# Performance work log

Measured on AMD Instinct MI355X. Metric: run time of the kernel, lower is better.

The kernel has to match this reference:

```python
import jax, jax.numpy as jnp
import numpy as np

HIDDEN = 2048
N_HEADS = 32
N_KV = 8
HEAD_DIM = 128
EPS = 1e-6
THETA = 10000.0
WINDOW = 512
T = 2048


def _rms_norm(x, w, eps=EPS):
    # x: [..., d]
    var = jnp.mean(x * x, axis=-1, keepdims=True)
    return x * jax.lax.rsqrt(var + eps) * w


def _rope(x, positions):
    # neox-style full rotary, x: [T, H, d]
    d = x.shape[-1]
    inv_freq = 1.0 / (THETA ** (jnp.arange(0, d, 2, dtype=jnp.float32) / d))  # [d/2]
    ang = positions.astype(jnp.float32)[:, None] * inv_freq  # [T, d/2]
    cos = jnp.cos(ang)[:, None, :]  # [T,1,d/2]
    sin = jnp.sin(ang)[:, None, :]
    x1, x2 = x[..., : d // 2], x[..., d // 2 :]
    return jnp.concatenate([x1 * cos - x2 * sin, x2 * cos + x1 * sin], axis=-1)


def setup_inputs() -> dict:
    key = jax.random.key(0)
    ks = jax.random.split(key, 6)
    q_size = N_HEADS * HEAD_DIM
    kv_size = N_KV * HEAD_DIM
    s = 1.0 / np.sqrt(HIDDEN)
    return {
        "positions": jnp.arange(T, dtype=jnp.int32),
        "hidden_states": jax.random.normal(ks[0], (T, HIDDEN), dtype=jnp.float32),
        "w_qkv": jax.random.normal(ks[1], (HIDDEN, q_size + 2 * kv_size), dtype=jnp.float32) * s,
        "w_o": jax.random.normal(ks[2], (q_size, HIDDEN), dtype=jnp.float32) * s,
        "w_g": jax.random.normal(ks[3], (HIDDEN, N_HEADS), dtype=jnp.float32) * s,
        "q_norm_w": jnp.ones((HEAD_DIM,), dtype=jnp.float32),
        "k_norm_w": jnp.ones((HEAD_DIM,), dtype=jnp.float32),
    }


def reference(positions, hidden_states, w_qkv, w_o, w_g, q_norm_w, k_norm_w):
    t = hidden_states.shape[0]
    q_size = N_HEADS * HEAD_DIM
    kv_size = N_KV * HEAD_DIM
    scale = HEAD_DIM ** -0.5
    group = N_HEADS // N_KV

    qkv = hidden_states @ w_qkv  # [T, q+2kv]
    q = qkv[:, :q_size].reshape(t, N_HEADS, HEAD_DIM)
    k = qkv[:, q_size : q_size + kv_size].reshape(t, N_KV, HEAD_DIM)
    v = qkv[:, q_size + kv_size :].reshape(t, N_KV, HEAD_DIM)

    # per-head RMSNorm then RoPE
    q = _rope(_rms_norm(q, q_norm_w), positions)
    k = _rope(_rms_norm(k, k_norm_w), positions)

    # sliding-window causal attention with GQA (group queries per kv head)
    qg = q.reshape(t, N_KV, group, HEAD_DIM)
    scores = jnp.einsum("tkgd,skd->kgts", qg, k) * scale  # [Hkv,G,T,T]
    diff = positions[:, None] - positions[None, :]  # i - j
    mask = (diff >= 0) & (diff < WINDOW)  # causal + sliding window
    scores = jnp.where(mask[None, None], scores, -jnp.inf)
    probs = jax.nn.softmax(scores, axis=-1)
    attn = jnp.einsum("kgts,skd->tkgd", probs, v).reshape(t, N_HEADS, HEAD_DIM)

    # softplus gate per head, then output projection
    gate = jax.nn.softplus((hidden_states @ w_g).astype(jnp.float32)).astype(attn.dtype)
    attn = attn * gate[:, :, None]
    return attn.reshape(t, q_size) @ w_o
```

## Files before the change

kernel.cpp:

```cpp
#include <hip/hip_runtime.h>

typedef __attribute__((ext_vector_type(4))) float floatx4;
typedef __attribute__((ext_vector_type(8))) _Float16 half8;
typedef __attribute__((ext_vector_type(4))) _Float16 half4;

#define TT 2048
#define HIDDEN 2048
#define NH 32
#define NKV 8
#define HD 128
#define QSIZE 4096
#define KVSIZE 1024
#define QKVN 6144
#define WQR 6400
#define GOFF 6144
#define QKSTR 5120
#define WINDOW 512

__global__ __launch_bounds__(256) void prep_kernel(
    const float* __restrict__ w_qkv, const float* __restrict__ w_o,
    const float* __restrict__ hidden, const float* __restrict__ w_g,
    const int* __restrict__ positions,
    _Float16* __restrict__ Wqkvt, _Float16* __restrict__ Wot,
    _Float16* __restrict__ Xb, float* __restrict__ tbl) {
  __shared__ float tile[64][68];
  int bid = blockIdx.x;
  int tid = threadIdx.x;
  if (bid >= 5120) {
    if (bid < 7168) {
      int i = ((bid - 5120) * 256 + tid) * 8;
      float4 a = *(const float4*)&hidden[i];
      float4 b = *(const float4*)&hidden[i + 4];
      alignas(16) _Float16 o[8] = {(_Float16)a.x, (_Float16)a.y, (_Float16)a.z, (_Float16)a.w,
                                   (_Float16)b.x, (_Float16)b.y, (_Float16)b.z, (_Float16)b.w};
      *(uint4*)&Xb[i] = *(const uint4*)o;
    } else if (bid < 7392) {
      int i = ((bid - 7168) * 256 + tid) * 8;
      *(uint4*)&Wqkvt[(size_t)(GOFF + NH) * HIDDEN + i] = (uint4){0, 0, 0, 0};
    } else if (bid < 7456) {
      int br = (bid - 7392) * 32;
      int c = tid & 31, r0 = tid >> 5;
      __shared__ float gt[32][33];
#pragma unroll
      for (int i = 0; i < 4; ++i) {
        int r = r0 + 8 * i;
        gt[r][c] = w_g[(size_t)(br + r) * NH + c];
      }
      __syncthreads();
#pragma unroll
      for (int i = 0; i < 4; ++i) {
        int r = r0 + 8 * i;
        Wqkvt[(size_t)(GOFF + r) * HIDDEN + br + c] = (_Float16)gt[c][r];
      }
    } else {
      int idx = (bid - 7456) * 256 + tid;
      int t = idx >> 6, j = idx & 63;
      float pos = (float)positions[t];
      float invf = exp2f(-(float)j * (13.287712379549449f / 64.0f));
      float sn, cs;
      sincosf(pos * invf, &sn, &cs);
      tbl[t * 128 + j] = cs;
      tbl[t * 128 + 64 + j] = sn;
    }
    return;
  }
  const float* in;
  _Float16* out;
  int R, C, tilesX, t;
  if (bid < 3072) { in = w_qkv; out = Wqkvt; R = HIDDEN; C = QKVN; tilesX = 96; t = bid; }
  else           { in = w_o;   out = Wot;   R = QSIZE;  C = HIDDEN; tilesX = 32; t = bid - 3072; }
  int bc = (t % tilesX) * 64, br = (t / tilesX) * 64;
  int rr = tid >> 4, l16 = tid & 15;
#pragma unroll
  for (int it = 0; it < 4; ++it) {
    int r = rr + it * 16;
    *(float4*)&tile[r][l16 * 4] = *(const float4*)&in[(size_t)(br + r) * C + bc + l16 * 4];
  }
  __syncthreads();
  int orow = tid >> 2, rr0 = (tid & 3) * 16;
  alignas(16) _Float16 tmp[16];
#pragma unroll
  for (int jj = 0; jj < 16; ++jj) tmp[jj] = (_Float16)tile[rr0 + jj][orow];
  *(uint4*)&out[(size_t)(bc + orow) * R + br + rr0] = *(const uint4*)&tmp[0];
  *(uint4*)&out[(size_t)(bc + orow) * R + br + rr0 + 8] = *(const uint4*)&tmp[8];
}

__device__ __forceinline__ void async16(const _Float16* g, _Float16* l) {
  __builtin_amdgcn_global_load_lds((const __attribute__((address_space(1))) void*)g,
                                   (__attribute__((address_space(3))) void*)l, 16, 0, 0);
}

#define G256_K 2048

#define STG_A(ob, mh, kt)                                                        \
  async16(As0 + (size_t)(mh) * 64 * G256_K + (kt), &lds[(ob) + ((mh) * 64 + r0A0) * 64]); \
  async16(As1 + (size_t)(mh) * 64 * G256_K + (kt), &lds[(ob) + ((mh) * 64 + r0A1) * 64]);
#define STG_B(ob, nh, kt)                                                        \
  async16(Bs0 + (size_t)(nh) * 32 * G256_K + (kt), &lds[(ob) + 16384 + ((nh) * 32 + r0B0) * 64]); \
  async16(Bs1 + (size_t)(nh) * 32 * G256_K + (kt), &lds[(ob) + 16384 + ((nh) * 32 + r0B1) * 64]);

#define LD_A(DST, mh)                                                            \
  _Pragma("unroll") for (int fm = 0; fm < 4; ++fm)                               \
  _Pragma("unroll") for (int ks = 0; ks < 2; ++ks)                               \
    DST[fm][ks] = *(const half8*)&LA[(wm * 128 + (mh) * 64 + fm * 16 + lr) * 64 + \
                                     (((ks * 4 + quad) ^ l7) * 8)];
#define LD_B(DST, nh)                                                            \
  _Pragma("unroll") for (int fn = 0; fn < 2; ++fn)                               \
  _Pragma("unroll") for (int ks = 0; ks < 2; ++ks)                               \
    DST[fn][ks] = *(const half8*)&LB[(wn * 64 + (nh) * 32 + fn * 16 + lr) * 64 + \
                                     (((ks * 4 + quad) ^ l7) * 8)];
#define MFMAQ(AS, BS, mh, nh)                                                    \
  __builtin_amdgcn_s_setprio(1);                                                 \
  _Pragma("unroll") for (int fm = 0; fm < 4; ++fm)                               \
  _Pragma("unroll") for (int fn = 0; fn < 2; ++fn)                               \
  _Pragma("unroll") for (int ks = 0; ks < 2; ++ks)                               \
    acc[(mh) * 4 + fm][(nh) * 2 + fn] = __builtin_amdgcn_mfma_f32_16x16x32_f16(  \
        AS[fm][ks], BS[fn][ks], acc[(mh) * 4 + fm][(nh) * 2 + fn], 0, 0, 0);     \
  __builtin_amdgcn_s_setprio(0);
#define VMW0 asm volatile("s_waitcnt vmcnt(0)" ::: "memory")
#define BAR __builtin_amdgcn_s_barrier()
#define SB0 __builtin_amdgcn_sched_barrier(0)

__global__ __launch_bounds__(512, 2) void gemm256_kernel(
    const _Float16* __restrict__ A, const _Float16* __restrict__ Bt,
    _Float16* __restrict__ QKb, _Float16* __restrict__ Vf,
    _Float16* __restrict__ Gate) {
  __shared__ _Float16 lds[65536];
  int tid = threadIdx.x;
  int wave = tid >> 6, lane = tid & 63;
  int wm = wave >> 2, wn = wave & 3;
  int lr = lane & 15, quad = lane >> 4, l7 = lane & 7, l3 = lane >> 3;
  int m0 = blockIdx.x * 256, n0 = blockIdx.y * 256;

  int q0 = wave * 2, q1 = q0 + 1;
  int r0A0 = (q0 >> 3) * 128 + (q0 & 7) * 8;
  int r0A1 = (q1 >> 3) * 128 + (q1 & 7) * 8;
  int r0B0 = (q0 >> 2) * 64 + (q0 & 3) * 8;
  int r0B1 = (q1 >> 2) * 64 + (q1 & 3) * 8;
  int gA8 = (l7 ^ l3) * 8;

  const _Float16* As0 = A + (size_t)(m0 + r0A0 + l3) * G256_K + gA8;
  const _Float16* As1 = A + (size_t)(m0 + r0A1 + l3) * G256_K + gA8;
  const _Float16* Bs0 = Bt + (size_t)(n0 + r0B0 + l3) * G256_K + gA8;
  const _Float16* Bs1 = Bt + (size_t)(n0 + r0B1 + l3) * G256_K + gA8;

  floatx4 acc[8][4];
#pragma unroll
  for (int i = 0; i < 8; ++i)
#pragma unroll
    for (int j = 0; j < 4; ++j) acc[i][j] = (floatx4){0.f, 0.f, 0.f, 0.f};

  STG_A(0, 0, 0);
  STG_A(0, 1, 0);
  STG_B(0, 0, 0);
  STG_B(0, 1, 0);
  VMW0;
  BAR;
  SB0;

  half8 a0f[4][2], a1f[4][2], b0[2][2], b1[2][2];

  for (int t = 0; t < 32; ++t) {
    int bb = (t & 1) << 15;
    int ob = bb ^ 32768;
    int ktn = (t + 1) * 64;
    bool stg = (t < 31);
    const _Float16* LA = &lds[bb];
    const _Float16* LB = &lds[bb + 16384];

    if (stg) {
      STG_A(ob, 0, ktn);
      STG_B(ob, 0, ktn);
      STG_B(ob, 1, ktn);
      STG_A(ob, 1, ktn);
    }

    LD_B(b0, 0);
    LD_A(a0f, 0);
    MFMAQ(a0f, b0, 0, 0);
    LD_B(b1, 1);
    MFMAQ(a0f, b1, 0, 1);
    LD_A(a1f, 1);
    MFMAQ(a1f, b0, 1, 0);
    MFMAQ(a1f, b1, 1, 1);

    if (stg) VMW0;
    BAR;
    SB0;
  }

  int nt = blockIdx.y;
  if (nt < 20) {
#pragma unroll
    for (int mh = 0; mh < 2; ++mh)
#pragma unroll
      for (int fm = 0; fm < 4; ++fm)
#pragma unroll
        for (int nh = 0; nh < 2; ++nh)
#pragma unroll
          for (int fn = 0; fn < 2; ++fn)
#pragma unroll
            for (int rr = 0; rr < 4; ++rr) {
              int row = m0 + wm * 128 + mh * 64 + fm * 16 + quad * 4 + rr;
              int col = nt * 256 + wn * 64 + nh * 32 + fn * 16 + lr;
              QKb[(size_t)row * QKSTR + col] = (_Float16)acc[mh * 4 + fm][nh * 2 + fn][rr];
            }
  } else if (nt < 24) {
#pragma unroll
    for (int mh = 0; mh < 2; ++mh)
#pragma unroll
      for (int fm = 0; fm < 4; ++fm)
#pragma unroll
        for (int nh = 0; nh < 2; ++nh)
#pragma unroll
          for (int fn = 0; fn < 2; ++fn)
#pragma unroll
            for (int rq = 0; rq < 4; ++rq) {
              int row = fm * 16 + quad * 4 + rq;
              int t = m0 + wm * 128 + mh * 64 + row;
              int cg = wn * 64 + nh * 32 + fn * 16 + lr;
              int kh = (nt - 20) * 2 + (cg >> 7);
              int d = cg & 127;
              int sv = t & 63;
              _Float16* vb = Vf + ((size_t)kh * 32 + (t >> 6)) * 8192;
              int c = (d >> 4) * 128 + (sv >> 5) * 64 + ((sv >> 3) & 3) * 16 + (d & 15);
              vb[c * 8 + (sv & 7)] = (_Float16)acc[mh * 4 + fm][nh * 2 + fn][rq];
            }
  } else {
    if (wn == 0) {
#pragma unroll
      for (int mh = 0; mh < 2; ++mh)
#pragma unroll
        for (int fm = 0; fm < 4; ++fm)
#pragma unroll
          for (int fn = 0; fn < 2; ++fn)
#pragma unroll
            for (int rq = 0; rq < 4; ++rq) {
              int row = fm * 16 + quad * 4 + rq;
              int t = m0 + wm * 128 + mh * 64 + row;
              int col = fn * 16 + lr;
              Gate[(size_t)t * NH + col] = (_Float16)acc[mh * 4 + fm][fn][rq];
            }
    }
  }
}

__global__ __launch_bounds__(256) void normrope_k_kernel(
    const _Float16* __restrict__ QKb, const float* __restrict__ kw,
    const float* __restrict__ tbl, _Float16* __restrict__ Kf) {
  int wid = blockIdx.x * 4 + (threadIdx.x >> 6);
  int lane = threadIdx.x & 63;
  int t = wid >> 3, hh = wid & 7;
  const _Float16* src = QKb + (size_t)t * QKSTR + QSIZE + hh * HD;
  float x1 = (float)src[lane];
  float x2 = (float)src[lane + 64];
  float ss = x1 * x1 + x2 * x2;
#pragma unroll
  for (int off = 1; off < 64; off <<= 1) ss += __shfl_xor(ss, off);
  float rr = rsqrtf(ss * (1.0f / 128.0f) + 1e-6f);
  float n1 = x1 * rr * kw[lane];
  float n2 = x2 * rr * kw[lane + 64];
  float cs = tbl[(size_t)t * 128 + lane];
  float sn = tbl[(size_t)t * 128 + 64 + lane];
  float r1 = n1 * cs - n2 * sn;
  float r2 = n2 * cs + n1 * sn;
  int st = t >> 6, jt = (t >> 4) & 3, n16 = t & 15;
  _Float16* kb = Kf + (size_t)(hh * 32 + st) * 8192;
  int c = jt * 256 + (lane >> 5) * 64 + ((lane >> 3) & 3) * 16 + n16;
  kb[c * 8 + (lane & 7)] = (_Float16)r1;
  kb[(c + 128) * 8 + (lane & 7)] = (_Float16)r2;
}

__device__ __forceinline__ void swizzle_mn(int& m0, int& n0) {
  int ntiles = gridDim.y;
  int pid = blockIdx.x + blockIdx.y * gridDim.x;
  int band = pid / (8 * ntiles);
  int wi = pid - band * (8 * ntiles);
  m0 = (band * 8 + (wi & 7)) * 128;
  n0 = (wi >> 3) * 128;
}

__global__ __launch_bounds__(256, 2) void gemm_bt_splitk_kernel(
    const _Float16* __restrict__ A, const _Float16* __restrict__ Bt,
    float* __restrict__ Cp, int M, int N, int K, int Ks) {
  __shared__ _Float16 As[128 * 64];
  __shared__ _Float16 Bs[128 * 64];
  int tid = threadIdx.x;
  int wave = tid >> 6, lane = tid & 63;
  int wm = wave >> 1, wn = wave & 1;
  int m0, n0;
  swizzle_mn(m0, n0);
  int kb = blockIdx.z * Ks;
  float* C = Cp + (size_t)blockIdx.z * M * N;
  int lr = lane & 15;
  int quad = lane >> 4;
  floatx4 acc[4][4];
#pragma unroll
  for (int i = 0; i < 4; ++i)
#pragma unroll
    for (int j = 0; j < 4; ++j) acc[i][j] = (floatx4){0.f, 0.f, 0.f, 0.f};

  for (int k0 = kb; k0 < kb + Ks; k0 += 64) {
    __syncthreads();
#pragma unroll
    for (int it = 0; it < 4; ++it) {
      int c = tid + it * 256;
      int row = c >> 3, j = c & 7;
      int jj = j ^ (row & 7);
      _Float16* la = &As[it * 2048 + wave * 512];
      _Float16* lb = &Bs[it * 2048 + wave * 512];
      async16(&A[(size_t)(m0 + row) * K + k0 + jj * 8], la);
      async16(&Bt[(size_t)(n0 + row) * K + k0 + jj * 8], lb);
    }
    __syncthreads();
#pragma unroll
    for (int kc = 0; kc < 2; ++kc) {
      int ch = kc * 4 + quad;
      half8 a[4], b[4];
#pragma unroll
      for (int i = 0; i < 4; ++i) {
        int r = wm * 64 + i * 16 + lr;
        a[i] = *(const half8*)&As[r * 64 + (ch ^ (r & 7)) * 8];
      }
#pragma unroll
      for (int j = 0; j < 4; ++j) {
        int r = wn * 64 + j * 16 + lr;
        b[j] = *(const half8*)&Bs[r * 64 + (ch ^ (r & 7)) * 8];
      }
#pragma unroll
      for (int i = 0; i < 4; ++i)
#pragma unroll
        for (int j = 0; j < 4; ++j)
          acc[i][j] = __builtin_amdgcn_mfma_f32_16x16x32_f16(a[i], b[j], acc[i][j], 0, 0, 0);
    }
  }
  int rq = quad * 4;
#pragma unroll
  for (int i = 0; i < 4; ++i)
#pragma unroll
    for (int j = 0; j < 4; ++j)
#pragma unroll
      for (int r = 0; r < 4; ++r) {
        int row = m0 + wm * 64 + i * 16 + rq + r;
        int col = n0 + wn * 64 + j * 16 + lr;
        C[(size_t)row * N + col] = acc[i][j][r];
      }
}

__global__ __launch_bounds__(256) void reduce2_kernel(const float* __restrict__ P,
                                                      float* __restrict__ out) {
  size_t i = ((size_t)blockIdx.x * 256 + threadIdx.x) * 8;
  const float* Q = P + (size_t)TT * HIDDEN;
  float4 a0 = *(const float4*)&P[i];
  float4 a1 = *(const float4*)&P[i + 4];
  float4 b0 = *(const float4*)&Q[i];
  float4 b1 = *(const float4*)&Q[i + 4];
  a0.x += b0.x; a0.y += b0.y; a0.z += b0.z; a0.w += b0.w;
  a1.x += b1.x; a1.y += b1.y; a1.z += b1.z; a1.w += b1.w;
  *(float4*)&out[i] = a0;
  *(float4*)&out[i + 4] = a1;
}

#define PSTR 68
#define M0 8.0f
__global__ __launch_bounds__(256, 2) void attn_kernel(
    const _Float16* __restrict__ QKb, const float* __restrict__ qw,
    const float* __restrict__ tbl, const _Float16* __restrict__ Kf,
    const _Float16* __restrict__ Vf, const _Float16* __restrict__ Gate,
    _Float16* __restrict__ Og) {
  const float scale = 0.08838834764831845f;
  __shared__ _Float16 Ps[4][16 * PSTR];
  int tid = threadIdx.x;
  int wave = tid >> 6, lane = tid & 63;
  int n16 = lane & 15, quad = lane >> 4;
  int t0 = blockIdx.x * 16;
  int kh = blockIdx.y;
  int h = kh * 4 + wave;
  _Float16* ps = Ps[wave];

  half8 qf[4];
  {
    int tq = t0 + n16;
    half8 rq[4];
#pragma unroll
    for (int kc = 0; kc < 4; ++kc)
      rq[kc] = *(const half8*)&QKb[(size_t)tq * QKSTR + h * HD + kc * 32 + quad * 8];
    float x[4][8];
    float ss = 0.f;
#pragma unroll
    for (int kc = 0; kc < 4; ++kc)
#pragma unroll
      for (int j = 0; j < 8; ++j) {
        x[kc][j] = (float)rq[kc][j];
        ss += x[kc][j] * x[kc][j];
      }
    ss += __shfl_xor(ss, 16);
    ss += __shfl_xor(ss, 32);
    float inv = rsqrtf(ss * (1.0f / 128.0f) + 1e-6f);
#pragma unroll
    for (int kc = 0; kc < 2; ++kc) {
      int d0 = kc * 32 + quad * 8;
      const float* tb = &tbl[(size_t)tq * 128 + d0];
      const float* w1 = &qw[d0];
      const float* w2 = &qw[d0 + 64];
#pragma unroll
      for (int j = 0; j < 8; ++j) {
        float cs = tb[j], sn = tb[64 + j];
        float x1 = x[kc][j] * inv * w1[j];
        float x2 = x[kc + 2][j] * inv * w2[j];
        qf[kc][j] = (_Float16)(x1 * cs - x2 * sn);
        qf[kc + 2][j] = (_Float16)(x2 * cs + x1 * sn);
      }
    }
  }

  floatx4 O[8];
  float lp[4];
#pragma unroll
  for (int jd = 0; jd < 8; ++jd) O[jd] = (floatx4){0.f, 0.f, 0.f, 0.f};
#pragma unroll
  for (int r = 0; r < 4; ++r) lp[r] = 0.f;

  int lo = t0 - (WINDOW - 1);
  if (lo < 0) lo = 0;
  int st0 = lo >> 6;
  int st1 = t0 >> 6;

  half8 kfr[4][4];
  {
    const _Float16* kb = Kf + (size_t)(kh * 32 + st0) * 8192;
#pragma unroll
    for (int jt = 0; jt < 4; ++jt)
#pragma unroll
      for (int kc = 0; kc < 4; ++kc)
        kfr[jt][kc] = *(const half8*)&kb[(jt * 4 + kc) * 512 + lane * 8];
  }

  for (int st = st0; st <= st1; ++st) {
    int s0 = st * 64;
    const _Float16* vb = Vf + (size_t)(kh * 32 + st) * 8192;
    floatx4 S[4];
#pragma unroll
    for (int jt = 0; jt < 4; ++jt) S[jt] = (floatx4){0.f, 0.f, 0.f, 0.f};
#pragma unroll
    for (int jt = 0; jt < 4; ++jt)
#pragma unroll
      for (int kc = 0; kc < 4; ++kc)
        S[jt] = __builtin_amdgcn_mfma_f32_16x16x32_f16(qf[kc], kfr[jt][kc], S[jt], 0, 0, 0);
    if (st < st1) {
      const _Float16* kb = Kf + (size_t)(kh * 32 + st + 1) * 8192;
#pragma unroll
      for (int jt = 0; jt < 4; ++jt)
#pragma unroll
        for (int kc = 0; kc < 4; ++kc)
          kfr[jt][kc] = *(const half8*)&kb[(jt * 4 + kc) * 512 + lane * 8];
    }
    bool interior = (t0 >= s0 + 63) && (t0 + 15 - s0 < WINDOW);
    if (interior) {
#pragma unroll
      for (int r = 0; r < 4; ++r) {
        float rs = 0.f;
#pragma unroll
        for (int jt = 0; jt < 4; ++jt) {
          float p = __expf(__builtin_fmaf(S[jt][r], scale, -M0));
          rs += p;
          ps[(quad * 4 + r) * PSTR + jt * 16 + n16] = (_Float16)p;
        }
        lp[r] += rs;
      }
    } else {
#pragma unroll
      for (int r = 0; r < 4; ++r) {
        int tq = t0 + quad * 4 + r;
        float rs = 0.f;
#pragma unroll
        for (int jt = 0; jt < 4; ++jt) {
          int diff = tq - (s0 + jt * 16 + n16);
          bool ok = (diff >= 0) && (diff < WINDOW);
          float p = ok ? __expf(__builtin_fmaf(S[jt][r], scale, -M0)) : 0.f;
          rs += p;
          ps[(quad * 4 + r) * PSTR + jt * 16 + n16] = (_Float16)p;
        }
        lp[r] += rs;
      }
    }
    half8 pf[2];
#pragma unroll
    for (int kc = 0; kc < 2; ++kc) {
      half4 lo4 = *(const half4*)&ps[n16 * PSTR + kc * 32 + quad * 8];
      half4 hi4 = *(const half4*)&ps[n16 * PSTR + kc * 32 + quad * 8 + 4];
      pf[kc] = (half8){lo4[0], lo4[1], lo4[2], lo4[3], hi4[0], hi4[1], hi4[2], hi4[3]};
    }
#pragma unroll
    for (int jd = 0; jd < 8; ++jd) {
#pragma unroll
      for (int kc = 0; kc < 2; ++kc) {
        half8 vfr = *(const half8*)&vb[(jd * 2 + kc) * 512 + lane * 8];
        O[jd] = __builtin_amdgcn_mfma_f32_16x16x32_f16(pf[kc], vfr, O[jd], 0, 0, 0);
      }
    }
  }
#pragma unroll
  for (int r = 0; r < 4; ++r) {
    float l = lp[r];
#pragma unroll
    for (int off = 1; off < 16; off <<= 1) l += __shfl_xor(l, off);
    int t = t0 + quad * 4 + r;
    float gl = (float)Gate[(size_t)t * NH + h];
    float g = (gl > 0.f) ? gl + log1pf(__expf(-gl)) : log1pf(__expf(gl));
    float inv = g / l;
#pragma unroll
    for (int jd = 0; jd < 8; ++jd)
      Og[(size_t)t * QSIZE + h * HD + jd * 16 + n16] = (_Float16)(O[jd][r] * inv);
  }
}

extern "C" void kernel_launch(void* const* d_in, const int* in_sizes, int n_in,
                              void* d_out, int out_size, void* d_ws, size_t ws_size,
                              hipStream_t stream) {
  const int* positions = (const int*)d_in[0];
  const float* hidden = (const float*)d_in[1];
  const float* w_qkv = (const float*)d_in[2];
  const float* w_o = (const float*)d_in[3];
  const float* w_g = (const float*)d_in[4];
  const float* q_norm_w = (const float*)d_in[5];
  const float* k_norm_w = (const float*)d_in[6];
  float* out = (float*)d_out;

  char* ws = (char*)d_ws;
  size_t off = 0;
  auto alloc = [&](size_t bytes) {
    void* p = ws + off;
    off += (bytes + 255) & ~(size_t)255;
    return p;
  };
  _Float16* Xb = (_Float16*)alloc((size_t)TT * HIDDEN * 2);
  _Float16* Wqkvt = (_Float16*)alloc((size_t)WQR * HIDDEN * 2);
  _Float16* Wot = (_Float16*)alloc((size_t)HIDDEN * QSIZE * 2);
  _Float16* QKb = (_Float16*)alloc((size_t)TT * QKSTR * 2);
  _Float16* Kf = (_Float16*)alloc((size_t)NKV * 32 * 8192 * 2);
  _Float16* Vf = (_Float16*)alloc((size_t)NKV * 32 * 8192 * 2);
  _Float16* Og = (_Float16*)alloc((size_t)TT * QSIZE * 2);
  _Float16* Gate = (_Float16*)alloc((size_t)TT * NH * 2);
  float* CosSin = (float*)alloc((size_t)TT * 128 * 4);
  float* Cp = (float*)ws;

  prep_kernel<<<7968, 256, 0, stream>>>(w_qkv, w_o, hidden, w_g, positions,
                                        Wqkvt, Wot, Xb, CosSin);
  gemm256_kernel<<<dim3(TT / 256, WQR / 256), 512, 0, stream>>>(
      Xb, Wqkvt, QKb, Vf, Gate);
  normrope_k_kernel<<<(TT * NKV) / 4, 256, 0, stream>>>(QKb, k_norm_w, CosSin, Kf);
  attn_kernel<<<dim3(TT / 16, NKV), 256, 0, stream>>>(QKb, q_norm_w, CosSin,
                                                      Kf, Vf, Gate, Og);
  gemm_bt_splitk_kernel<<<dim3(TT / 128, HIDDEN / 128, 2), 256, 0, stream>>>(
      Og, Wot, Cp, TT, HIDDEN, QSIZE, QSIZE / 2);
  reduce2_kernel<<<(TT * HIDDEN) / (256 * 8), 256, 0, stream>>>(Cp, out);
}
```

Measured before the change: 302.1 us.

## Replace split-K output GEMM and reduce with single full-K 128x64 tile GEMM

The output projection previously split K in two, wrote fp32 partial results for each half, and summed them in a separate reduce kernel. It now uses one GEMM with 128x64 tiles over the full K that writes directly to the output, keeping the same block count. This removes the partial-buffer write/read traffic and an extra launch. In exchange each block does more K iterations with lower per-tile reuse, and the L2-friendly block swizzle is dropped.

```diff
diff --git a/kernel.cpp b/kernel.cpp
--- a/kernel.cpp
+++ b/kernel.cpp
@@ -271,64 +271,54 @@
   kb[(c + 128) * 8 + (lane & 7)] = (_Float16)r2;
 }
 
-__device__ __forceinline__ void swizzle_mn(int& m0, int& n0) {
-  int ntiles = gridDim.y;
-  int pid = blockIdx.x + blockIdx.y * gridDim.x;
-  int band = pid / (8 * ntiles);
-  int wi = pid - band * (8 * ntiles);
-  m0 = (band * 8 + (wi & 7)) * 128;
-  n0 = (wi >> 3) * 128;
-}
-
-__global__ __launch_bounds__(256, 2) void gemm_bt_splitk_kernel(
+__global__ __launch_bounds__(256, 2) void gemm_o_kernel(
     const _Float16* __restrict__ A, const _Float16* __restrict__ Bt,
-    float* __restrict__ Cp, int M, int N, int K, int Ks) {
+    float* __restrict__ C) {
   __shared__ _Float16 As[128 * 64];
-  __shared__ _Float16 Bs[128 * 64];
+  __shared__ _Float16 Bs[64 * 64];
   int tid = threadIdx.x;
   int wave = tid >> 6, lane = tid & 63;
-  int wm = wave >> 1, wn = wave & 1;
-  int m0, n0;
-  swizzle_mn(m0, n0);
-  int kb = blockIdx.z * Ks;
-  float* C = Cp + (size_t)blockIdx.z * M * N;
-  int lr = lane & 15;
-  int quad = lane >> 4;
-  floatx4 acc[4][4];
-#pragma unroll
-  for (int i = 0; i < 4; ++i)
+  int m0 = blockIdx.x * 128, n0 = blockIdx.y * 64;
+  int lr = lane & 15, quad = lane >> 4;
+  floatx4 acc[2][4];
+#pragma unroll
+  for (int i = 0; i < 2; ++i)
 #pragma unroll
     for (int j = 0; j < 4; ++j) acc[i][j] = (floatx4){0.f, 0.f, 0.f, 0.f};
 
-  for (int k0 = kb; k0 < kb + Ks; k0 += 64) {
+  for (int k0 = 0; k0 < QSIZE; k0 += 64) {
     __syncthreads();
 #pragma unroll
     for (int it = 0; it < 4; ++it) {
       int c = tid + it * 256;
       int row = c >> 3, j = c & 7;
       int jj = j ^ (row & 7);
-      _Float16* la = &As[it * 2048 + wave * 512];
-      _Float16* lb = &Bs[it * 2048 + wave * 512];
-      async16(&A[(size_t)(m0 + row) * K + k0 + jj * 8], la);
-      async16(&Bt[(size_t)(n0 + row) * K + k0 + jj * 8], lb);
+      async16(&A[(size_t)(m0 + row) * QSIZE + k0 + jj * 8], &As[it * 2048 + wave * 512]);
+    }
+#pragma unroll
+    for (int it = 0; it < 2; ++it) {
+      int c = tid + it * 256;
+      int row = c >> 3, j = c & 7;
+      int jj = j ^ (row & 7);
+      async16(&Bt[(size_t)(n0 + row) * QSIZE + k0 + jj * 8], &Bs[it * 2048 + wave * 512]);
     }
     __syncthreads();
 #pragma unroll
     for (int kc = 0; kc < 2; ++kc) {
       int ch = kc * 4 + quad;
-      half8 a[4], b[4];
-#pragma unroll
-      for (int i = 0; i < 4; ++i) {
-        int r = wm * 64 + i * 16 + lr;
+      half8 a[2], b[4];
+#pragma unroll
+      for (int i = 0; i < 2; ++i) {
+        int r = wave * 32 + i * 16 + lr;
         a[i] = *(const half8*)&As[r * 64 + (ch ^ (r & 7)) * 8];
       }
 #pragma unroll
       for (int j = 0; j < 4; ++j) {
-        int r = wn * 64 + j * 16 + lr;
+        int r = j * 16 + lr;
         b[j] = *(const half8*)&Bs[r * 64 + (ch ^ (r & 7)) * 8];
       }
 #pragma unroll
-      for (int i = 0; i < 4; ++i)
+      for (int i = 0; i < 2; ++i)
 #pragma unroll
         for (int j = 0; j < 4; ++j)
           acc[i][j] = __builtin_amdgcn_mfma_f32_16x16x32_f16(a[i], b[j], acc[i][j], 0, 0, 0);
@@ -336,29 +326,15 @@
   }
   int rq = quad * 4;
 #pragma unroll
-  for (int i = 0; i < 4; ++i)
+  for (int i = 0; i < 2; ++i)
 #pragma unroll
     for (int j = 0; j < 4; ++j)
 #pragma unroll
       for (int r = 0; r < 4; ++r) {
-        int row = m0 + wm * 64 + i * 16 + rq + r;
-        int col = n0 + wn * 64 + j * 16 + lr;
-        C[(size_t)row * N + col] = acc[i][j][r];
-      }
-}
-
-__global__ __launch_bounds__(256) void reduce2_kernel(const float* __restrict__ P,
-                                                      float* __restrict__ out) {
-  size_t i = ((size_t)blockIdx.x * 256 + threadIdx.x) * 8;
-  const float* Q = P + (size_t)TT * HIDDEN;
-  float4 a0 = *(const float4*)&P[i];
-  float4 a1 = *(const float4*)&P[i + 4];
-  float4 b0 = *(const float4*)&Q[i];
-  float4 b1 = *(const float4*)&Q[i + 4];
-  a0.x += b0.x; a0.y += b0.y; a0.z += b0.z; a0.w += b0.w;
-  a1.x += b1.x; a1.y += b1.y; a1.z += b1.z; a1.w += b1.w;
-  *(float4*)&out[i] = a0;
-  *(float4*)&out[i + 4] = a1;
+        int row = m0 + wave * 32 + i * 16 + rq + r;
+        int col = n0 + j * 16 + lr;
+        C[(size_t)row * HIDDEN + col] = acc[i][j][r];
+      }
 }
 
 #define PSTR 68
@@ -543,7 +519,6 @@
   _Float16* Og = (_Float16*)alloc((size_t)TT * QSIZE * 2);
   _Float16* Gate = (_Float16*)alloc((size_t)TT * NH * 2);
   float* CosSin = (float*)alloc((size_t)TT * 128 * 4);
-  float* Cp = (float*)ws;
 
   prep_kernel<<<7968, 256, 0, stream>>>(w_qkv, w_o, hidden, w_g, positions,
                                         Wqkvt, Wot, Xb, CosSin);
@@ -552,7 +527,5 @@
   normrope_k_kernel<<<(TT * NKV) / 4, 256, 0, stream>>>(QKb, k_norm_w, CosSin, Kf);
   attn_kernel<<<dim3(TT / 16, NKV), 256, 0, stream>>>(QKb, q_norm_w, CosSin,
                                                       Kf, Vf, Gate, Og);
-  gemm_bt_splitk_kernel<<<dim3(TT / 128, HIDDEN / 128, 2), 256, 0, stream>>>(
-      Og, Wot, Cp, TT, HIDDEN, QSIZE, QSIZE / 2);
-  reduce2_kernel<<<(TT * HIDDEN) / (256 * 8), 256, 0, stream>>>(Cp, out);
-}
+  gemm_o_kernel<<<dim3(TT / 128, HIDDEN / 64), 256, 0, stream>>>(Og, Wot, out);
+}
```

Measured after the change: 304.3 us. About the same (+0.7%).

## Stage K/V tiles in double-buffered LDS via async copies in attention

Applied to the files above, without the earlier changes.

The attention kernel now copies each 64-key K and V tile into shared memory with async global-to-LDS loads, using two buffers so the next tile is fetched while the current one is computed. Before, each of the four waves (one per query head in the GQA group) loaded identical K/V fragments straight from global memory into registers. Sharing one copy across the waves cuts redundant global traffic and register pressure. In exchange it adds 64KB of LDS per block, which may limit occupancy below the two blocks per CU requested by launch bounds, and a block barrier on every iteration.

```diff
diff --git a/kernel.cpp b/kernel.cpp
--- a/kernel.cpp
+++ b/kernel.cpp
@@ -369,6 +369,7 @@
     const _Float16* __restrict__ Vf, const _Float16* __restrict__ Gate,
     _Float16* __restrict__ Og) {
   const float scale = 0.08838834764831845f;
+  __shared__ _Float16 KV[2][16384];
   __shared__ _Float16 Ps[4][16 * PSTR];
   int tid = threadIdx.x;
   int wave = tid >> 6, lane = tid & 63;
@@ -378,6 +379,21 @@
   int h = kh * 4 + wave;
   _Float16* ps = Ps[wave];
 
+  int lo = t0 - (WINDOW - 1);
+  if (lo < 0) lo = 0;
+  int st0 = lo >> 6;
+  int st1 = t0 >> 6;
+
+  {
+    const _Float16* kb = Kf + (size_t)(kh * 32 + st0) * 8192;
+    const _Float16* vb = Vf + (size_t)(kh * 32 + st0) * 8192;
+#pragma unroll
+    for (int it = 0; it < 4; ++it) {
+      async16(kb + ((size_t)it * 256 + tid) * 8, &KV[0][it * 2048 + wave * 512]);
+      async16(vb + ((size_t)it * 256 + tid) * 8, &KV[0][8192 + it * 2048 + wave * 512]);
+    }
+  }
+
   half8 qf[4];
   {
     int tq = t0 + n16;
@@ -421,40 +437,36 @@
 #pragma unroll
   for (int r = 0; r < 4; ++r) lp[r] = 0.f;
 
-  int lo = t0 - (WINDOW - 1);
-  if (lo < 0) lo = 0;
-  int st0 = lo >> 6;
-  int st1 = t0 >> 6;
-
-  half8 kfr[4][4];
-  {
-    const _Float16* kb = Kf + (size_t)(kh * 32 + st0) * 8192;
+  VMW0;
+  BAR;
+  SB0;
+
+  for (int st = st0; st <= st1; ++st) {
+    int b = (st - st0) & 1;
+    const _Float16* Kb = KV[b];
+    const _Float16* Vb = KV[b] + 8192;
+    bool stg = (st < st1);
+    if (stg) {
+      const _Float16* kb = Kf + (size_t)(kh * 32 + st + 1) * 8192;
+      const _Float16* vb = Vf + (size_t)(kh * 32 + st + 1) * 8192;
+      int ob = b ^ 1;
+#pragma unroll
+      for (int it = 0; it < 4; ++it) {
+        async16(kb + ((size_t)it * 256 + tid) * 8, &KV[ob][it * 2048 + wave * 512]);
+        async16(vb + ((size_t)it * 256 + tid) * 8, &KV[ob][8192 + it * 2048 + wave * 512]);
+      }
+    }
+    int s0 = st * 64;
+    floatx4 S[4];
+#pragma unroll
+    for (int jt = 0; jt < 4; ++jt) S[jt] = (floatx4){0.f, 0.f, 0.f, 0.f};
 #pragma unroll
     for (int jt = 0; jt < 4; ++jt)
 #pragma unroll
-      for (int kc = 0; kc < 4; ++kc)
-        kfr[jt][kc] = *(const half8*)&kb[(jt * 4 + kc) * 512 + lane * 8];
-  }
-
-  for (int st = st0; st <= st1; ++st) {
-    int s0 = st * 64;
-    const _Float16* vb = Vf + (size_t)(kh * 32 + st) * 8192;
-    floatx4 S[4];
-#pragma unroll
-    for (int jt = 0; jt < 4; ++jt) S[jt] = (floatx4){0.f, 0.f, 0.f, 0.f};
-#pragma unroll
-    for (int jt = 0; jt < 4; ++jt)
-#pragma unroll
-      for (int kc = 0; kc < 4; ++kc)
-        S[jt] = __builtin_amdgcn_mfma_f32_16x16x32_f16(qf[kc], kfr[jt][kc], S[jt], 0, 0, 0);
-    if (st < st1) {
-      const _Float16* kb = Kf + (size_t)(kh * 32 + st + 1) * 8192;
-#pragma unroll
-      for (int jt = 0; jt < 4; ++jt)
-#pragma unroll
-        for (int kc = 0; kc < 4; ++kc)
-          kfr[jt][kc] = *(const half8*)&kb[(jt * 4 + kc) * 512 + lane * 8];
-    }
+      for (int kc = 0; kc < 4; ++kc) {
+        half8 kfr = *(const half8*)&Kb[(jt * 4 + kc) * 512 + lane * 8];
+        S[jt] = __builtin_amdgcn_mfma_f32_16x16x32_f16(qf[kc], kfr, S[jt], 0, 0, 0);
+      }
     bool interior = (t0 >= s0 + 63) && (t0 + 15 - s0 < WINDOW);
     if (interior) {
 #pragma unroll
@@ -495,10 +507,13 @@
     for (int jd = 0; jd < 8; ++jd) {
 #pragma unroll
       for (int kc = 0; kc < 2; ++kc) {
-        half8 vfr = *(const half8*)&vb[(jd * 2 + kc) * 512 + lane * 8];
+        half8 vfr = *(const half8*)&Vb[(jd * 2 + kc) * 512 + lane * 8];
         O[jd] = __builtin_amdgcn_mfma_f32_16x16x32_f16(pf[kc], vfr, O[jd], 0, 0, 0);
       }
     }
+    if (stg) VMW0;
+    BAR;
+    SB0;
   }
 #pragma unroll
   for (int r = 0; r < 4; ++r) {
```

After: 298.5 us. No clear change (-1.2%).
